# Kernel optimization log

Hardware: AMD Instinct MI355X
Metric: run time of the kernel (lower is better)

Reference implementation:

```python
import jax, jax.numpy as jnp
import numpy as np

N = 1_000_000   # detections
FDIM = 64       # embedding dim
C = 128         # number of clusters (track ids in [0, C))
DELTA_VAR = 0.5
DELTA_DIST = 3.0


def setup_inputs() -> dict:
    key = jax.random.key(0)
    k1, k2 = jax.random.split(key)
    features = jax.random.normal(k1, (N, FDIM), dtype=jnp.float32)
    labels = jax.random.randint(k2, (N, 2), 0, C, dtype=jnp.int32)  # [fr, track_id], all ids >= 0
    return {"features": features, "labels": labels}


def reference(features, labels):
    # All track ids are >= 0 by construction, so the tp_ids filter is a no-op
    # and the dynamic unique-cluster loop becomes a fixed-C segment reduce.
    ids = labels[:, 1]
    ones = jnp.ones((features.shape[0],), dtype=features.dtype)
    counts = jax.ops.segment_sum(ones, ids, num_segments=C)            # (C,)
    sums = jax.ops.segment_sum(features, ids, num_segments=C)         # (C, F)
    means = sums / counts[:, None]                                     # per-cluster mean

    # variance term: per-point distance to its cluster mean, hinged at delta_var
    d = jnp.linalg.norm(features - means[ids], axis=1)                 # (N,)
    per_pt = jnp.square(jax.nn.relu(d - DELTA_VAR))
    per_cluster = jax.ops.segment_sum(per_pt, ids, num_segments=C) / counts
    var_loss = jnp.sum(per_cluster) / C

    # pairwise cluster-distance term over i != j, hinged at delta_dist
    diff = means[:, None, :] - means[None, :, :]                       # (C, C, F)
    sq = jnp.sum(diff * diff, axis=-1)                                 # (C, C)
    eye = jnp.eye(C, dtype=bool)
    pd = jnp.sqrt(jnp.where(eye, 1.0, sq))                             # safe sqrt on diagonal
    dl = jnp.where(eye, 0.0, jnp.square(jax.nn.relu(DELTA_DIST - pd)))
    dist_loss = jnp.sum(dl) / (C * (C - 1))

    return var_loss + dist_loss
```

## Files before the change

kernel.cpp:

```cpp
#include <hip/hip_runtime.h>

#define NPTS 1000000
#define FDIM 64
#define CNUM 128
#define PSTRIDE 8320
#define NB1 512
#define NB3 1024

typedef _Float16 half8 __attribute__((ext_vector_type(8)));
typedef float f32x4 __attribute__((ext_vector_type(4)));

__global__ __launch_bounds__(256, 2) void k1_partials(
    const float* __restrict__ feats, const int* __restrict__ labels,
    float* __restrict__ partials, int nblocks)
{
    __shared__ float lds[CNUM * 65];
    __shared__ float cnt[CNUM];
    const int tid = threadIdx.x;
    if (tid < CNUM) cnt[tid] = 0.f;
    __syncthreads();

    const int lane = tid & 63;
    const int n15 = lane & 15;
    const int kb = (lane >> 4) * 8;
    const int nwaves = nblocks * 4;
    const int wid = ((blockIdx.x << 8) + tid) >> 6;

    f32x4 acc[8][4];
    #pragma unroll
    for (int ct = 0; ct < 8; ++ct)
        #pragma unroll
        for (int nt = 0; nt < 4; ++nt)
            acc[ct][nt] = (f32x4){0.f, 0.f, 0.f, 0.f};

    const int ntiles = NPTS / 32;
    for (int t = wid; t < ntiles; t += nwaves) {
        const int p0 = t * 32;
        int vlab[8];
        #pragma unroll
        for (int i = 0; i < 8; ++i)
            vlab[i] = labels[2 * (p0 + kb + i) + 1];
        const int myl = labels[2 * (p0 + (lane & 31)) + 1];
        if (lane < 32) atomicAdd(&cnt[myl], 1.0f);

        half8 B[4];
        #pragma unroll
        for (int nt = 0; nt < 4; ++nt) {
            #pragma unroll
            for (int i = 0; i < 8; ++i) {
                float v = feats[(size_t)(p0 + kb + i) * FDIM + nt * 16 + n15];
                B[nt][i] = (_Float16)v;
            }
        }
        #pragma unroll
        for (int ct = 0; ct < 8; ++ct) {
            const int cmine = ct * 16 + n15;
            union { unsigned u[4]; half8 h; } ua;
            #pragma unroll
            for (int j = 0; j < 4; ++j)
                ua.u[j] = ((vlab[2 * j] == cmine) ? 0x3C00u : 0u)
                        | ((vlab[2 * j + 1] == cmine) ? 0x3C000000u : 0u);
            #pragma unroll
            for (int nt = 0; nt < 4; ++nt)
                acc[ct][nt] = __builtin_amdgcn_mfma_f32_16x16x32_f16(
                    ua.h, B[nt], acc[ct][nt], 0, 0, 0);
        }
    }
    __syncthreads();

    const int w = tid >> 6;
    const int rowb = (lane >> 4) * 4;
    for (int r = 0; r < 4; ++r) {
        if (w == r) {
            #pragma unroll
            for (int ct = 0; ct < 8; ++ct)
                #pragma unroll
                for (int nt = 0; nt < 4; ++nt)
                    #pragma unroll
                    for (int reg = 0; reg < 4; ++reg) {
                        const int c = ct * 16 + rowb + reg;
                        const int f = nt * 16 + n15;
                        if (r == 0) lds[c * 65 + f] = acc[ct][nt][reg];
                        else        lds[c * 65 + f] += acc[ct][nt][reg];
                    }
        }
        __syncthreads();
    }

    float* dst = partials + (size_t)blockIdx.x * PSTRIDE;
    for (int i = tid; i < 8192; i += 256)
        dst[i] = lds[(i >> 6) * 65 + (i & 63)];
    if (tid < CNUM) dst[8192 + tid] = cnt[tid];
}

__global__ __launch_bounds__(256) void k2_reduce(
    const float* __restrict__ partials, int nblocks, float* __restrict__ red)
{
    const int t = (blockIdx.x % 33) * 256 + threadIdx.x;
    const int s = blockIdx.x / 33;
    if (t >= PSTRIDE) return;
    float sum = 0.f;
    #pragma unroll 4
    for (int b = s; b < nblocks; b += 4)
        sum += partials[(size_t)b * PSTRIDE + t];
    atomicAdd(&red[t], sum);
}

__global__ __launch_bounds__(256, 4) void k3_var(
    const float4* __restrict__ feats4, const int* __restrict__ labels,
    const float* __restrict__ red, float* __restrict__ ppsum, int nblocks)
{
    __shared__ float4 mu4[CNUM * 16];
    __shared__ float lpp[CNUM];
    const int tid = threadIdx.x;
    for (int i = tid; i < 2048; i += 256) {
        float4 sv = ((const float4*)red)[i];
        float ci = 1.0f / red[8192 + (i >> 4)];
        mu4[i] = make_float4(sv.x * ci, sv.y * ci, sv.z * ci, sv.w * ci);
    }
    if (tid < CNUM) lpp[tid] = 0.f;
    __syncthreads();

    const int lane = tid & 63;
    const int k = lane & 15, g = lane >> 4;
    const int nwaves = nblocks * 4;
    const int wid = ((blockIdx.x << 8) + tid) >> 6;

    for (int b = wid; b < NPTS / 32; b += nwaves) {
        const int p0 = b * 32;
        float4 v[8];
        #pragma unroll
        for (int s = 0; s < 8; ++s)
            v[s] = feats4[(size_t)(p0 + 4 * s) * 16 + lane];
        const int cc = labels[2 * (p0 + (lane & 31)) + 1];

        #pragma unroll
        for (int s = 0; s < 8; ++s) {
            const int c = __shfl(cc, 4 * s + g);
            float4 m = mu4[c * 16 + k];
            float dx = v[s].x - m.x, dy = v[s].y - m.y,
                  dz = v[s].z - m.z, dw = v[s].w - m.w;
            float sq = dx * dx + dy * dy + dz * dz + dw * dw;
            sq += __shfl_xor(sq, 1); sq += __shfl_xor(sq, 2);
            sq += __shfl_xor(sq, 4); sq += __shfl_xor(sq, 8);
            if (k == 0) {
                const float t = sqrtf(sq) - 0.5f;
                if (t > 0.f) atomicAdd(&lpp[c], t * t);
            }
        }
    }
    __syncthreads();
    if (tid < CNUM) atomicAdd(&ppsum[tid], lpp[tid]);
}

__global__ __launch_bounds__(128) void k4_dist(
    const float* __restrict__ red, float* __restrict__ dsum)
{
    __shared__ float4 mu4[CNUM * 17];
    const int tid = threadIdx.x;
    for (int i = tid; i < 2048; i += 128) {
        float4 sv = ((const float4*)red)[i];
        float ci = 1.0f / red[8192 + (i >> 4)];
        mu4[(i >> 4) * 17 + (i & 15)] =
            make_float4(sv.x * ci, sv.y * ci, sv.z * ci, sv.w * ci);
    }
    __syncthreads();
    const int i = blockIdx.x, j = tid;
    float sq = 0.f;
    #pragma unroll
    for (int q = 0; q < 16; ++q) {
        float4 a = mu4[i * 17 + q], b = mu4[j * 17 + q];
        float dx = a.x - b.x, dy = a.y - b.y, dz = a.z - b.z, dw = a.w - b.w;
        sq += dx * dx + dy * dy + dz * dz + dw * dw;
    }
    float dl = 0.f;
    if (j != i) {
        const float r = 3.0f - sqrtf(sq);
        if (r > 0.f) dl = r * r;
    }
    #pragma unroll
    for (int m = 1; m < 64; m <<= 1) dl += __shfl_xor(dl, m);
    if ((tid & 63) == 0) atomicAdd(dsum, dl);
}

__global__ __launch_bounds__(128) void k5_final(
    const float* __restrict__ red, const float* __restrict__ ppsum,
    const float* __restrict__ dsum, float* __restrict__ out)
{
    const int t = threadIdx.x;
    float v = ppsum[t] / red[8192 + t];
    #pragma unroll
    for (int m = 1; m < 64; m <<= 1) v += __shfl_xor(v, m);
    __shared__ float sv[2];
    if ((t & 63) == 0) sv[t >> 6] = v;
    __syncthreads();
    if (t == 0)
        out[0] = (sv[0] + sv[1]) / (float)CNUM
               + dsum[0] / (float)(CNUM * (CNUM - 1));
}

extern "C" void kernel_launch(void* const* d_in, const int* in_sizes, int n_in,
                              void* d_out, int out_size, void* d_ws, size_t ws_size,
                              hipStream_t stream) {
    (void)in_sizes; (void)n_in; (void)out_size;
    const float* feats   = (const float*)d_in[0];
    const float4* feats4 = (const float4*)d_in[0];
    const int* labels    = (const int*)d_in[1];
    float* ws            = (float*)d_ws;
    float* out           = (float*)d_out;

    int nb1 = NB1;
    {
        size_t avail = ws_size / sizeof(float);
        size_t fixed = PSTRIDE + 128 + 1;
        if (avail > fixed) {
            size_t cap = (avail - fixed) / PSTRIDE;
            if ((size_t)nb1 > cap) nb1 = (int)cap;
        } else nb1 = 1;
        if (nb1 < 1) nb1 = 1;
    }
    float* partials = ws;
    float* red      = ws + (size_t)nb1 * PSTRIDE;
    float* ppsum    = red + PSTRIDE;
    float* dsum     = ppsum + 128;

    hipMemsetAsync(red, 0, (PSTRIDE + CNUM + 1) * sizeof(float), stream);

    k1_partials<<<nb1, 256, 0, stream>>>(feats, labels, partials, nb1);
    k2_reduce<<<33 * 4, 256, 0, stream>>>(partials, nb1, red);
    k3_var<<<NB3, 256, 0, stream>>>(feats4, labels, red, ppsum, NB3);
    k4_dist<<<CNUM, 128, 0, stream>>>(red, dsum);
    k5_final<<<1, 128, 0, stream>>>(red, ppsum, dsum, out);
}
```

Baseline: 160.6 us.

## Fuse count into MFMA, drop memset and final kernel, prefetch in variance pass

Per-cluster counts are now computed by an extra MFMA against a ones vector instead of LDS atomics. The cross-wave LDS merge uses a transposed layout with vector stores. The reduction kernel writes results directly instead of using atomics, which removes the memset, and it zeroes the accumulators. The variance kernel double-buffers its global loads. The distance and final kernels are merged with a last-block counter pattern. Together these cut launch count and serialization, in exchange for more registers and a grid-wide completion counter.

After: 163.5 us. About the same (+1.8%).

```diff
diff --git a/kernel.cpp b/kernel.cpp
--- a/kernel.cpp
+++ b/kernel.cpp
@@ -14,43 +14,45 @@
     const float* __restrict__ feats, const int* __restrict__ labels,
     float* __restrict__ partials, int nblocks)
 {
-    __shared__ float lds[CNUM * 65];
-    __shared__ float cnt[CNUM];
-    const int tid = threadIdx.x;
-    if (tid < CNUM) cnt[tid] = 0.f;
-    __syncthreads();
-
+    __shared__ float lds[FDIM * 132];
+    __shared__ float cntw[4][130];
+    const int tid = threadIdx.x;
     const int lane = tid & 63;
     const int n15 = lane & 15;
     const int kb = (lane >> 4) * 8;
+    const int rowb = (lane >> 4) * 4;
+    const int w = tid >> 6;
     const int nwaves = nblocks * 4;
     const int wid = ((blockIdx.x << 8) + tid) >> 6;
 
     f32x4 acc[8][4];
-    #pragma unroll
-    for (int ct = 0; ct < 8; ++ct)
+    f32x4 accc[8];
+    #pragma unroll
+    for (int ct = 0; ct < 8; ++ct) {
+        accc[ct] = (f32x4){0.f, 0.f, 0.f, 0.f};
         #pragma unroll
         for (int nt = 0; nt < 4; ++nt)
             acc[ct][nt] = (f32x4){0.f, 0.f, 0.f, 0.f};
+    }
+    half8 B1;
+    #pragma unroll
+    for (int j = 0; j < 8; ++j) B1[j] = (_Float16)1.0f;
 
     const int ntiles = NPTS / 32;
     for (int t = wid; t < ntiles; t += nwaves) {
         const int p0 = t * 32;
+        const float* fp = feats + (size_t)(p0 + kb) * FDIM + n15;
+        const int* lp = labels + 2 * (p0 + kb) + 1;
         int vlab[8];
         #pragma unroll
-        for (int i = 0; i < 8; ++i)
-            vlab[i] = labels[2 * (p0 + kb + i) + 1];
-        const int myl = labels[2 * (p0 + (lane & 31)) + 1];
-        if (lane < 32) atomicAdd(&cnt[myl], 1.0f);
+        for (int i = 0; i < 8; ++i) vlab[i] = lp[2 * i];
 
         half8 B[4];
         #pragma unroll
         for (int nt = 0; nt < 4; ++nt) {
             #pragma unroll
-            for (int i = 0; i < 8; ++i) {
-                float v = feats[(size_t)(p0 + kb + i) * FDIM + nt * 16 + n15];
-                B[nt][i] = (_Float16)v;
-            }
+            for (int i = 0; i < 8; ++i)
+                B[nt][i] = (_Float16)fp[i * FDIM + nt * 16];
         }
         #pragma unroll
         for (int ct = 0; ct < 8; ++ct) {
@@ -64,46 +66,74 @@
             for (int nt = 0; nt < 4; ++nt)
                 acc[ct][nt] = __builtin_amdgcn_mfma_f32_16x16x32_f16(
                     ua.h, B[nt], acc[ct][nt], 0, 0, 0);
-        }
-    }
-    __syncthreads();
-
-    const int w = tid >> 6;
-    const int rowb = (lane >> 4) * 4;
+            accc[ct] = __builtin_amdgcn_mfma_f32_16x16x32_f16(
+                ua.h, B1, accc[ct], 0, 0, 0);
+        }
+    }
+
+    if (n15 == 0) {
+        #pragma unroll
+        for (int ct = 0; ct < 8; ++ct)
+            #pragma unroll
+            for (int reg = 0; reg < 4; ++reg)
+                cntw[w][ct * 16 + rowb + reg] = accc[ct][reg];
+    }
+
     for (int r = 0; r < 4; ++r) {
-        if (w == r) {
-            #pragma unroll
-            for (int ct = 0; ct < 8; ++ct)
-                #pragma unroll
-                for (int nt = 0; nt < 4; ++nt)
-                    #pragma unroll
-                    for (int reg = 0; reg < 4; ++reg) {
-                        const int c = ct * 16 + rowb + reg;
-                        const int f = nt * 16 + n15;
-                        if (r == 0) lds[c * 65 + f] = acc[ct][nt][reg];
-                        else        lds[c * 65 + f] += acc[ct][nt][reg];
-                    }
+        const int q = (w + r) & 3;
+        #pragma unroll
+        for (int c2 = 0; c2 < 2; ++c2) {
+            const int ct = 2 * q + c2;
+            #pragma unroll
+            for (int nt = 0; nt < 4; ++nt) {
+                float* a = &lds[(nt * 16 + n15) * 132 + ct * 16 + rowb];
+                if (r == 0) {
+                    *(f32x4*)a = acc[ct][nt];
+                } else {
+                    f32x4 old = *(f32x4*)a;
+                    *(f32x4*)a = old + acc[ct][nt];
+                }
+            }
         }
         __syncthreads();
     }
 
     float* dst = partials + (size_t)blockIdx.x * PSTRIDE;
-    for (int i = tid; i < 8192; i += 256)
-        dst[i] = lds[(i >> 6) * 65 + (i & 63)];
-    if (tid < CNUM) dst[8192 + tid] = cnt[tid];
+    for (int i4 = tid; i4 < 2048; i4 += 256) {
+        const int f = i4 >> 5, c0 = (i4 & 31) * 4;
+        ((float4*)dst)[i4] = *(float4*)&lds[f * 132 + c0];
+    }
+    if (tid < CNUM)
+        dst[8192 + tid] = cntw[0][tid] + cntw[1][tid] + cntw[2][tid] + cntw[3][tid];
 }
 
 __global__ __launch_bounds__(256) void k2_reduce(
-    const float* __restrict__ partials, int nblocks, float* __restrict__ red)
-{
-    const int t = (blockIdx.x % 33) * 256 + threadIdx.x;
-    const int s = blockIdx.x / 33;
-    if (t >= PSTRIDE) return;
-    float sum = 0.f;
-    #pragma unroll 4
-    for (int b = s; b < nblocks; b += 4)
-        sum += partials[(size_t)b * PSTRIDE + t];
-    atomicAdd(&red[t], sum);
+    const float* __restrict__ partials, int nblocks, float* __restrict__ red,
+    float* __restrict__ ppsum, float* __restrict__ dsum, int* __restrict__ counter)
+{
+    const int tid = threadIdx.x;
+    const int tsub = tid & 31, grp = tid >> 5;
+    const int t0 = blockIdx.x * 32;
+    float s = 0.f;
+    #pragma unroll 8
+    for (int b = grp; b < nblocks; b += 8)
+        s += partials[(size_t)b * PSTRIDE + t0 + tsub];
+    __shared__ float lred[8][33];
+    lred[grp][tsub] = s;
+    __syncthreads();
+    if (tid < 32) {
+        float tot = 0.f;
+        #pragma unroll
+        for (int q = 0; q < 8; ++q) tot += lred[q][tid];
+        const int t = t0 + tid;
+        if (t < 8192) red[(t & 127) * FDIM + (t >> 7)] = tot;
+        else red[t] = tot;
+    }
+    if (blockIdx.x == 0) {
+        if (tid >= 128) ppsum[tid - 128] = 0.f;
+        if (tid == 64) dsum[0] = 0.f;
+        if (tid == 65) counter[0] = 0;
+    }
 }
 
 __global__ __launch_bounds__(256, 4) void k3_var(
@@ -125,15 +155,25 @@
     const int k = lane & 15, g = lane >> 4;
     const int nwaves = nblocks * 4;
     const int wid = ((blockIdx.x << 8) + tid) >> 6;
-
-    for (int b = wid; b < NPTS / 32; b += nwaves) {
-        const int p0 = b * 32;
-        float4 v[8];
-        #pragma unroll
-        for (int s = 0; s < 8; ++s)
-            v[s] = feats4[(size_t)(p0 + 4 * s) * 16 + lane];
-        const int cc = labels[2 * (p0 + (lane & 31)) + 1];
-
+    const int ntiles = NPTS / 32;
+
+    int b = wid;
+    float4 v[8]; int cc = 0;
+    if (b < ntiles) {
+        const float4* fp = feats4 + (size_t)b * 512 + lane;
+        #pragma unroll
+        for (int s = 0; s < 8; ++s) v[s] = fp[s * 64];
+        cc = labels[2 * (b * 32 + (lane & 31)) + 1];
+    }
+    while (b < ntiles) {
+        const int bn = b + nwaves;
+        float4 vn[8]; int ccn = 0;
+        if (bn < ntiles) {
+            const float4* fp = feats4 + (size_t)bn * 512 + lane;
+            #pragma unroll
+            for (int s = 0; s < 8; ++s) vn[s] = fp[s * 64];
+            ccn = labels[2 * (bn * 32 + (lane & 31)) + 1];
+        }
         #pragma unroll
         for (int s = 0; s < 8; ++s) {
             const int c = __shfl(cc, 4 * s + g);
@@ -148,21 +188,28 @@
                 if (t > 0.f) atomicAdd(&lpp[c], t * t);
             }
         }
+        b = bn;
+        #pragma unroll
+        for (int s = 0; s < 8; ++s) v[s] = vn[s];
+        cc = ccn;
     }
     __syncthreads();
     if (tid < CNUM) atomicAdd(&ppsum[tid], lpp[tid]);
 }
 
-__global__ __launch_bounds__(128) void k4_dist(
-    const float* __restrict__ red, float* __restrict__ dsum)
+__global__ __launch_bounds__(128) void k45_dist_final(
+    const float* __restrict__ red, const float* __restrict__ ppsum,
+    float* __restrict__ dsum, int* __restrict__ counter, float* __restrict__ out)
 {
     __shared__ float4 mu4[CNUM * 17];
+    __shared__ int lastflag;
+    __shared__ float sv[2];
     const int tid = threadIdx.x;
     for (int i = tid; i < 2048; i += 128) {
-        float4 sv = ((const float4*)red)[i];
+        float4 s4 = ((const float4*)red)[i];
         float ci = 1.0f / red[8192 + (i >> 4)];
         mu4[(i >> 4) * 17 + (i & 15)] =
-            make_float4(sv.x * ci, sv.y * ci, sv.z * ci, sv.w * ci);
+            make_float4(s4.x * ci, s4.y * ci, s4.z * ci, s4.w * ci);
     }
     __syncthreads();
     const int i = blockIdx.x, j = tid;
@@ -181,22 +228,22 @@
     #pragma unroll
     for (int m = 1; m < 64; m <<= 1) dl += __shfl_xor(dl, m);
     if ((tid & 63) == 0) atomicAdd(dsum, dl);
-}
-
-__global__ __launch_bounds__(128) void k5_final(
-    const float* __restrict__ red, const float* __restrict__ ppsum,
-    const float* __restrict__ dsum, float* __restrict__ out)
-{
-    const int t = threadIdx.x;
-    float v = ppsum[t] / red[8192 + t];
-    #pragma unroll
-    for (int m = 1; m < 64; m <<= 1) v += __shfl_xor(v, m);
-    __shared__ float sv[2];
-    if ((t & 63) == 0) sv[t >> 6] = v;
-    __syncthreads();
-    if (t == 0)
+    __threadfence();
+    __syncthreads();
+    if (tid == 0) lastflag = (atomicAdd(counter, 1) == (int)gridDim.x - 1);
+    __syncthreads();
+    if (lastflag) {
+        float v = ppsum[tid] / red[8192 + tid];
+        #pragma unroll
+        for (int m = 1; m < 64; m <<= 1) v += __shfl_xor(v, m);
+        if ((tid & 63) == 0) sv[tid >> 6] = v;
+    }
+    __syncthreads();
+    if (lastflag && tid == 0) {
+        const float dtot = atomicAdd(dsum, 0.0f);
         out[0] = (sv[0] + sv[1]) / (float)CNUM
-               + dsum[0] / (float)(CNUM * (CNUM - 1));
+               + dtot / (float)(CNUM * (CNUM - 1));
+    }
 }
 
 extern "C" void kernel_launch(void* const* d_in, const int* in_sizes, int n_in,
@@ -212,7 +259,7 @@
     int nb1 = NB1;
     {
         size_t avail = ws_size / sizeof(float);
-        size_t fixed = PSTRIDE + 128 + 1;
+        size_t fixed = PSTRIDE + 128 + 2;
         if (avail > fixed) {
             size_t cap = (avail - fixed) / PSTRIDE;
             if ((size_t)nb1 > cap) nb1 = (int)cap;
@@ -223,12 +270,10 @@
     float* red      = ws + (size_t)nb1 * PSTRIDE;
     float* ppsum    = red + PSTRIDE;
     float* dsum     = ppsum + 128;
-
-    hipMemsetAsync(red, 0, (PSTRIDE + CNUM + 1) * sizeof(float), stream);
+    int*   counter  = (int*)(dsum + 1);
 
     k1_partials<<<nb1, 256, 0, stream>>>(feats, labels, partials, nb1);
-    k2_reduce<<<33 * 4, 256, 0, stream>>>(partials, nb1, red);
+    k2_reduce<<<PSTRIDE / 32, 256, 0, stream>>>(partials, nb1, red, ppsum, dsum, counter);
     k3_var<<<NB3, 256, 0, stream>>>(feats4, labels, red, ppsum, NB3);
-    k4_dist<<<CNUM, 128, 0, stream>>>(red, dsum);
-    k5_final<<<1, 128, 0, stream>>>(red, ppsum, dsum, out);
-}
+    k45_dist_final<<<CNUM, 128, 0, stream>>>(red, ppsum, dsum, counter, out);
+}
```
